# Optimization experiments

Hardware: AMD Instinct MI355X
Metric: run time of the kernel (lower is better)

The kernel has to match this reference:

```python
import jax, jax.numpy as jnp
import numpy as np

B, S, D = 8, 4096, 64

def setup_inputs() -> dict:
    key = jax.random.key(0)
    k1, k2 = jax.random.split(key)
    x = jax.random.normal(k1, (B, S, D), dtype=jnp.float32)
    y = jax.random.normal(k2, (B, S, D), dtype=jnp.float32)
    return {"x": x, "y": y}

def reference(x, y):
    # Unscaled bidirectional cross-attention.
    # m1: [B, Sx, Sy] = x @ y^T ; m2: [B, Sy, Sx] = y @ x^T (= m1^T, but keep faithful form)
    m1 = jnp.einsum('bsd,btd->bst', x, y)
    m2 = jnp.einsum('btd,bsd->bts', y, x)
    n1 = jax.nn.softmax(m1, axis=-1)
    n2 = jax.nn.softmax(m2, axis=-1)
    o1 = jnp.einsum('bst,btd->bsd', n1, y)
    o2 = jnp.einsum('bts,bsd->btd', n2, x)
    a1 = o1 * x
    a2 = o2 * y
    return jnp.concatenate((a1, a2), axis=-1)  # [B, S, 2D]
```

## Files before the change

kernel.cpp:

```cpp
#include <hip/hip_runtime.h>
#include <stdint.h>
#include <stddef.h>

#define SS 4096
#define DD 64
#define TK 64
#define NEG_M_L2 (-57.70780163555854f)
#define SQRT_L2E 1.2011224087864498f

typedef short    short4v __attribute__((ext_vector_type(4)));
typedef short    short8 __attribute__((ext_vector_type(8)));
typedef _Float16 half8  __attribute__((ext_vector_type(8)));
typedef float    f32x4  __attribute__((ext_vector_type(4)));
typedef __bf16   bf16x4v __attribute__((ext_vector_type(4)));
typedef __bf16   bf16x8v __attribute__((ext_vector_type(8)));
typedef __bf16   bf16x8 __attribute__((ext_vector_type(8)));

typedef __attribute__((address_space(1))) void void_g;
typedef __attribute__((address_space(3))) void void_l;

static __device__ __forceinline__ void gl_lds16(const void* g, void* l) {
    __builtin_amdgcn_global_load_lds((void_g*)(g), (void_l*)(l), 16, 0, 0);
}
static __device__ __forceinline__ float bf16_to_f32(unsigned short h) {
    uint32_t u = ((uint32_t)h) << 16;
    return __builtin_bit_cast(float, u);
}

#define MFMA_F16(A, B, C) __builtin_amdgcn_mfma_f32_16x16x32_f16( \
    __builtin_bit_cast(half8, A), __builtin_bit_cast(half8, B), (C), 0, 0, 0)
#define MFMA_BF16(A, B, C) __builtin_amdgcn_mfma_f32_16x16x32_bf16( \
    __builtin_bit_cast(bf16x8, A), __builtin_bit_cast(bf16x8, B), (C), 0, 0, 0)

__global__ __launch_bounds__(256) void prep(
    const float* __restrict__ x, const float* __restrict__ y,
    _Float16* __restrict__ fx, _Float16* __restrict__ fy,
    unsigned short* __restrict__ tx, unsigned short* __restrict__ ty) {
    __shared__ float tile[64 * 69];
    int bid = blockIdx.x;
    int mat = bid >> 9;
    int rem = bid & 511;
    int b = rem >> 6, t64 = rem & 63;
    int s0 = t64 * 64;
    const float* src = (mat ? y : x) + ((size_t)b * SS + s0) * 64;
    _Float16* fr = (mat ? fy : fx) + ((size_t)b * SS + s0) * 64;
    unsigned short* tr = (mat ? ty : tx) + (size_t)b * SS * 64;
    int tid = threadIdx.x;
#pragma unroll
    for (int it = 0; it < 4; ++it) {
        int qi = it * 256 + tid;
        int r = qi >> 4, c4 = (qi & 15) * 4;
        f32x4 v = *(const f32x4*)(src + r * 64 + c4);
#pragma unroll
        for (int j = 0; j < 4; ++j) tile[r * 69 + c4 + j] = v[j];
    }
#pragma unroll
    for (int j2 = 0; j2 < 2; ++j2) {
        int seg = j2 * 256 + tid;
        int r = seg >> 3, g = seg & 7;
        const float* sp8 = src + r * 64 + g * 8;
        f32x4 v0 = *(const f32x4*)(sp8);
        f32x4 v1 = *(const f32x4*)(sp8 + 4);
        half8 h;
#pragma unroll
        for (int j = 0; j < 4; ++j) {
            h[j]     = (_Float16)(v0[j] * SQRT_L2E);
            h[4 + j] = (_Float16)(v1[j] * SQRT_L2E);
        }
        *(half8*)(fr + (size_t)r * 64 + ((g + r + 2 * ((r >> 3) & 3)) & 7) * 8) = h;
    }
    __syncthreads();
#pragma unroll
    for (int j2 = 0; j2 < 2; ++j2) {
        int seg = j2 * 256 + tid;
        int d = seg >> 3, k8 = seg & 7;
        bf16x8v h;
#pragma unroll
        for (int i = 0; i < 8; ++i)
            h[i] = (__bf16)tile[(k8 * 8 + i) * 69 + d];
        *(short8*)(tr + (size_t)d * SS + s0 + ((k8 + d) & 7) * 8) =
            __builtin_bit_cast(short8, h);
    }
}

__global__ __launch_bounds__(256, 4)
void biattn(const float* __restrict__ xg, const float* __restrict__ yg,
            const _Float16* __restrict__ fx, const _Float16* __restrict__ fy,
            const unsigned short* __restrict__ tx, const unsigned short* __restrict__ ty,
            unsigned short* __restrict__ wsO, float* __restrict__ wsL,
            float* __restrict__ out, int mode) {
    __shared__ _Float16 shK[2][TK * DD];
    __shared__ unsigned short shVt[2][DD * TK];

    const int bid = blockIdx.x;
    const int g8 = bid >> 3;
    int half, bd, qb;
    qb = g8 & 31;
    if (mode) { half = (g8 >> 5) & 1; bd = (bid & 7) + 8 * (g8 >> 6); }
    else      { half = 0;             bd = (bid & 7) + 8 * (g8 >> 5); }
    const int b = bd >> 1, dir = bd & 1;
    const size_t mo = (size_t)b * SS * DD;
    const _Float16* Kf = (dir ? fx : fy) + mo;
    const unsigned short* Vt = (dir ? tx : ty) + mo;
    const _Float16* Qf = (dir ? fy : fx) + mo;
    const float* Qm = (dir ? yg : xg) + mo;

    const int tid = threadIdx.x, w = tid >> 6, ln = tid & 63;
    const int l15 = ln & 15, quad = ln >> 4;
    const int q0 = qb * 128 + w * 32;

    half8 qf[2][2];
#pragma unroll
    for (int qs = 0; qs < 2; ++qs) {
        int qrow = q0 + qs * 16 + l15;
#pragma unroll
        for (int c = 0; c < 2; ++c)
            qf[qs][c] = *(const half8*)(Qf + (size_t)qrow * 64 +
                ((c * 4 + quad + qrow + 2 * ((qrow >> 3) & 3)) & 7) * 8);
    }

    int koff[2][2][2];
#pragma unroll
    for (int c32 = 0; c32 < 2; ++c32)
#pragma unroll
        for (int st = 0; st < 2; ++st) {
            int kl = c32 * 32 + (l15 >> 2) * 8 + (l15 & 3) + st * 4;
            int rot = kl + 2 * ((kl >> 3) & 3);
#pragma unroll
            for (int c = 0; c < 2; ++c)
                koff[c32][st][c] = kl * 64 + ((c * 4 + quad + rot) & 7) * 8;
        }
    int rotv[2];
#pragma unroll
    for (int c32 = 0; c32 < 2; ++c32)
        rotv[c32] = ((c32 * 4 + quad + l15) & 7) * 8;

    const f32x4 negc4 = {NEG_M_L2, NEG_M_L2, NEG_M_L2, NEG_M_L2};
    const f32x4 zero4 = {0.f, 0.f, 0.f, 0.f};
    f32x4 Oa[2][4], La[2];
#pragma unroll
    for (int qs = 0; qs < 2; ++qs) {
        La[qs] = zero4;
#pragma unroll
        for (int dt = 0; dt < 4; ++dt) Oa[qs][dt] = zero4;
    }
    short8 onesb;
#pragma unroll
    for (int j = 0; j < 8; ++j) onesb[j] = (short)0x3F80;

    const int kblo = mode ? half * (SS / 2) : 0;
    const int kbhi = mode ? kblo + (SS / 2) : SS;

#define STAGE(BUF, KB) do {                                                   \
    _Pragma("unroll")                                                         \
    for (int i_ = 0; i_ < 4; ++i_) {                                          \
        int seg_ = w * 4 + i_;                            \
        if (seg_ < 8) {                                                       \
            gl_lds16(Kf + (size_t)(KB) * 64 + seg_ * 512 + ln * 8,            \
                     (void*)(&shK[(BUF)][0] + seg_ * 512));                   \
        } else {                                                              \
            int s2_ = seg_ - 8;                                               \
            int d_ = s2_ * 8 + (ln >> 3);                                     \
            gl_lds16(Vt + (size_t)d_ * SS + (KB) + (ln & 7) * 8,              \
                     (void*)(&shVt[(BUF)][0] + s2_ * 512));                   \
        }                                                                     \
    } } while (0)

    STAGE(0, kblo);
    __syncthreads();

    int buf = 0;
    for (int kb = kblo; kb < kbhi; kb += TK) {
        const int more = (kb + TK < kbhi);
        if (more) STAGE(buf ^ 1, kb + TK);
        const _Float16* Kb = &shK[buf][0];
        const unsigned short* Vb = &shVt[buf][0];

#pragma unroll
        for (int c32 = 0; c32 < 2; ++c32) {
            f32x4 sacc[2][2];
#pragma unroll
            for (int st = 0; st < 2; ++st) {
                half8 a0 = *(const half8*)(Kb + koff[c32][st][0]);
                half8 a1 = *(const half8*)(Kb + koff[c32][st][1]);
#pragma unroll
                for (int qs = 0; qs < 2; ++qs) {
                    f32x4 acc = MFMA_F16(a0, qf[qs][0], negc4);
                    sacc[qs][st] = MFMA_F16(a1, qf[qs][1], acc);
                }
            }
            short8 bfr[2];
#pragma unroll
            for (int qs = 0; qs < 2; ++qs) {
                bf16x8v pk;
#pragma unroll
                for (int st = 0; st < 2; ++st) {
                    f32x4 sv = sacc[qs][st];
#pragma unroll
                    for (int j = 0; j < 4; ++j)
                        pk[st * 4 + j] = (__bf16)__builtin_amdgcn_exp2f(sv[j]);
                }
                bfr[qs] = __builtin_bit_cast(short8, pk);
            }
#pragma unroll
            for (int dt = 0; dt < 4; ++dt) {
                short8 av = *(const short8*)(Vb + (dt * 16 + l15) * 64 + rotv[c32]);
                Oa[0][dt] = MFMA_BF16(av, bfr[0], Oa[0][dt]);
                Oa[1][dt] = MFMA_BF16(av, bfr[1], Oa[1][dt]);
            }
            La[0] = MFMA_BF16(onesb, bfr[0], La[0]);
            La[1] = MFMA_BF16(onesb, bfr[1], La[1]);
        }

        if (more) __syncthreads();
        buf ^= 1;
    }
#undef STAGE

    if (mode) {
        const int pb = half * 512 + bd * 32 + qb;
#pragma unroll
        for (int qs = 0; qs < 2; ++qs) {
            unsigned short* base = wsO + (size_t)pb * 8192
                                 + (size_t)(w * 2 + qs) * 1024 + l15 * 16 + quad * 4;
#pragma unroll
            for (int dt = 0; dt < 4; ++dt) {
                bf16x4v pk;
#pragma unroll
                for (int j = 0; j < 4; ++j) pk[j] = (__bf16)Oa[qs][dt][j];
                *(short4v*)(base + dt * 256) = __builtin_bit_cast(short4v, pk);
            }
            if (quad == 0)
                wsL[(size_t)pb * 128 + w * 32 + qs * 16 + l15] = La[qs][0];
        }
    } else {
#pragma unroll
        for (int qs = 0; qs < 2; ++qs) {
            float inv = 1.0f / La[qs][0];
            int qrow = q0 + qs * 16 + l15;
#pragma unroll
            for (int dt = 0; dt < 4; ++dt) {
                const float* qp = Qm + (size_t)qrow * DD + dt * 16 + quad * 4;
                f32x4 xv = *(const f32x4*)qp;
                f32x4 rr;
#pragma unroll
                for (int j = 0; j < 4; ++j) rr[j] = Oa[qs][dt][j] * inv * xv[j];
                float* op = out + ((size_t)(b * SS + qrow)) * 128 + dir * 64
                          + dt * 16 + quad * 4;
                *(f32x4*)op = rr;
            }
        }
    }
}

__global__ __launch_bounds__(256) void combine(
    const float* __restrict__ xg, const float* __restrict__ yg,
    const unsigned short* __restrict__ wsO, const float* __restrict__ wsL,
    float* __restrict__ out) {
    __shared__ float t[8 * 1088];
    int pb = blockIdx.x;
    int bd = pb >> 5, qb = pb & 31;
    int b = bd >> 1, dir = bd & 1;
    const unsigned short* p0 = wsO + (size_t)pb * 8192;
    const unsigned short* p1 = wsO + (size_t)(512 + pb) * 8192;
    const float* l0 = wsL + (size_t)pb * 128;
    const float* l1 = wsL + (size_t)(512 + pb) * 128;
    const float* Qm = (dir ? yg : xg) + (size_t)b * SS * DD;
    int tid = threadIdx.x;
#pragma unroll
    for (int j = 0; j < 8; ++j) {
        int idx = j * 1024 + tid * 4;
        short4v a = *(const short4v*)(p0 + idx);
        short4v c = *(const short4v*)(p1 + idx);
        int dt = (idx >> 8) & 3, q = (idx >> 4) & 15, dq = idx & 15;
#pragma unroll
        for (int jj = 0; jj < 4; ++jj)
            t[j * 1088 + (dt * 16 + dq + jj) * 17 + q] =
                bf16_to_f32((unsigned short)a[jj]) +
                bf16_to_f32((unsigned short)c[jj]);
    }
    __syncthreads();
    int w2 = tid >> 6, ln = tid & 63;
    int q00 = qb * 128;
#pragma unroll 4
    for (int i = 0; i < 32; ++i) {
        int q128 = w2 * 32 + i;
        int seg = q128 >> 4, lq = q128 & 15;
        float o = t[seg * 1088 + ln * 17 + lq];
        float l = l0[q128] + l1[q128];
        float qv = Qm[(size_t)(q00 + q128) * 64 + ln];
        out[((size_t)(b * SS + q00 + q128)) * 128 + dir * 64 + ln]
            = o * (1.0f / l) * qv;
    }
}

extern "C" void kernel_launch(void* const* d_in, const int* in_sizes, int n_in,
                              void* d_out, int out_size, void* d_ws, size_t ws_size,
                              hipStream_t stream) {
    const float* x = (const float*)d_in[0];
    const float* y = (const float*)d_in[1];
    char* ws = (char*)d_ws;
    const size_t MATB = (size_t)8 * SS * DD * 2;
    const size_t OSET = (size_t)1024 * 8192 * 2;
    const size_t LSET = (size_t)1024 * 128 * 4;
    _Float16* fx = (_Float16*)(ws);
    _Float16* fy = (_Float16*)(ws + MATB);
    unsigned short* tx = (unsigned short*)(ws + 2 * MATB);
    unsigned short* ty = (unsigned short*)(ws + 3 * MATB);
    unsigned short* wsO = (unsigned short*)(ws + 4 * MATB);
    float* wsL = (float*)(ws + 4 * MATB + OSET);
    const size_t need = 4 * MATB + OSET + LSET;
    const int mode = (ws_size >= need) ? 1 : 0;
    (void)in_sizes; (void)n_in; (void)out_size;
    prep<<<dim3(1024), dim3(256), 0, stream>>>(x, y, fx, fy, tx, ty);
    biattn<<<dim3(mode ? 1024 : 512), dim3(256), 0, stream>>>(
        x, y, fx, fy, tx, ty, wsO, wsL, (float*)d_out, mode);
    if (mode)
        combine<<<dim3(512), dim3(256), 0, stream>>>(x, y, wsO, wsL, (float*)d_out);
}
```

Before: 149.9 us.

## Use 512-thread blocks with 256 queries each and split keys four ways

The attention kernel now runs 8 waves per block covering 256 query rows, so each staged K/V tile is shared by twice as many queries. Keys are split into four chunks instead of two to keep the block count at 1024, and the combine kernel sums four bf16 partials and four row sums. The aim is to halve K/V staging traffic per query while keeping the GPU occupied. In exchange, the partial workspace doubles, combine reads more data, and the larger blocks may lower occupancy under the launch bound.

```diff
diff --git a/kernel.cpp b/kernel.cpp
--- a/kernel.cpp
+++ b/kernel.cpp
@@ -83,21 +83,20 @@
     }
 }
 
-__global__ __launch_bounds__(256, 4)
+__global__ __launch_bounds__(512, 4)
 void biattn(const float* __restrict__ xg, const float* __restrict__ yg,
             const _Float16* __restrict__ fx, const _Float16* __restrict__ fy,
             const unsigned short* __restrict__ tx, const unsigned short* __restrict__ ty,
             unsigned short* __restrict__ wsO, float* __restrict__ wsL,
-            float* __restrict__ out, int mode) {
+            float* __restrict__ out, int mode, int kcount) {
     __shared__ _Float16 shK[2][TK * DD];
     __shared__ unsigned short shVt[2][DD * TK];
 
     const int bid = blockIdx.x;
-    const int g8 = bid >> 3;
-    int half, bd, qb;
-    qb = g8 & 31;
-    if (mode) { half = (g8 >> 5) & 1; bd = (bid & 7) + 8 * (g8 >> 6); }
-    else      { half = 0;             bd = (bid & 7) + 8 * (g8 >> 5); }
+    const int s = mode ? (bid >> 8) : 0;
+    const int rr = bid & 255;
+    const int bd = (rr & 7) + 8 * (rr >> 7);
+    const int qt = (rr >> 3) & 15;
     const int b = bd >> 1, dir = bd & 1;
     const size_t mo = (size_t)b * SS * DD;
     const _Float16* Kf = (dir ? fx : fy) + mo;
@@ -107,7 +106,7 @@
 
     const int tid = threadIdx.x, w = tid >> 6, ln = tid & 63;
     const int l15 = ln & 15, quad = ln >> 4;
-    const int q0 = qb * 128 + w * 32;
+    const int q0 = qt * 256 + w * 32;
 
     half8 qf[2][2];
 #pragma unroll
@@ -148,13 +147,13 @@
 #pragma unroll
     for (int j = 0; j < 8; ++j) onesb[j] = (short)0x3F80;
 
-    const int kblo = mode ? half * (SS / 2) : 0;
-    const int kbhi = mode ? kblo + (SS / 2) : SS;
+    const int kblo = s * kcount;
+    const int kbhi = kblo + kcount;
 
 #define STAGE(BUF, KB) do {                                                   \
     _Pragma("unroll")                                                         \
-    for (int i_ = 0; i_ < 4; ++i_) {                                          \
-        int seg_ = w * 4 + i_;                            \
+    for (int i_ = 0; i_ < 2; ++i_) {                                          \
+        int seg_ = w * 2 + i_;                                                \
         if (seg_ < 8) {                                                       \
             gl_lds16(Kf + (size_t)(KB) * 64 + seg_ * 512 + ln * 8,            \
                      (void*)(&shK[(BUF)][0] + seg_ * 512));                   \
@@ -218,10 +217,10 @@
 #undef STAGE
 
     if (mode) {
-        const int pb = half * 512 + bd * 32 + qb;
+        const int ps = s * 256 + bd * 16 + qt;
 #pragma unroll
         for (int qs = 0; qs < 2; ++qs) {
-            unsigned short* base = wsO + (size_t)pb * 8192
+            unsigned short* base = wsO + (size_t)ps * 16384
                                  + (size_t)(w * 2 + qs) * 1024 + l15 * 16 + quad * 4;
 #pragma unroll
             for (int dt = 0; dt < 4; ++dt) {
@@ -231,7 +230,7 @@
                 *(short4v*)(base + dt * 256) = __builtin_bit_cast(short4v, pk);
             }
             if (quad == 0)
-                wsL[(size_t)pb * 128 + w * 32 + qs * 16 + l15] = La[qs][0];
+                wsL[(size_t)ps * 256 + w * 32 + qs * 16 + l15] = La[qs][0];
         }
     } else {
 #pragma unroll
@@ -242,12 +241,12 @@
             for (int dt = 0; dt < 4; ++dt) {
                 const float* qp = Qm + (size_t)qrow * DD + dt * 16 + quad * 4;
                 f32x4 xv = *(const f32x4*)qp;
-                f32x4 rr;
-#pragma unroll
-                for (int j = 0; j < 4; ++j) rr[j] = Oa[qs][dt][j] * inv * xv[j];
+                f32x4 rr2;
+#pragma unroll
+                for (int j = 0; j < 4; ++j) rr2[j] = Oa[qs][dt][j] * inv * xv[j];
                 float* op = out + ((size_t)(b * SS + qrow)) * 128 + dir * 64
                           + dt * 16 + quad * 4;
-                *(f32x4*)op = rr;
+                *(f32x4*)op = rr2;
             }
         }
     }
@@ -259,35 +258,41 @@
     float* __restrict__ out) {
     __shared__ float t[8 * 1088];
     int pb = blockIdx.x;
-    int bd = pb >> 5, qb = pb & 31;
+    int bd = pb >> 5, qb128 = pb & 31;
+    int qt = qb128 >> 1, hb = qb128 & 1;
     int b = bd >> 1, dir = bd & 1;
-    const unsigned short* p0 = wsO + (size_t)pb * 8192;
-    const unsigned short* p1 = wsO + (size_t)(512 + pb) * 8192;
-    const float* l0 = wsL + (size_t)pb * 128;
-    const float* l1 = wsL + (size_t)(512 + pb) * 128;
+    const size_t setO = (size_t)(bd * 16 + qt) * 16384 + (size_t)hb * 8192;
+    const size_t setL = (size_t)(bd * 16 + qt) * 256 + (size_t)hb * 128;
     const float* Qm = (dir ? yg : xg) + (size_t)b * SS * DD;
     int tid = threadIdx.x;
 #pragma unroll
     for (int j = 0; j < 8; ++j) {
         int idx = j * 1024 + tid * 4;
-        short4v a = *(const short4v*)(p0 + idx);
-        short4v c = *(const short4v*)(p1 + idx);
+        f32x4 a = {0.f, 0.f, 0.f, 0.f};
+#pragma unroll
+        for (int sp = 0; sp < 4; ++sp) {
+            short4v c = *(const short4v*)(wsO + (size_t)sp * 256 * 16384 + setO + idx);
+#pragma unroll
+            for (int jj = 0; jj < 4; ++jj)
+                a[jj] += bf16_to_f32((unsigned short)c[jj]);
+        }
         int dt = (idx >> 8) & 3, q = (idx >> 4) & 15, dq = idx & 15;
 #pragma unroll
         for (int jj = 0; jj < 4; ++jj)
-            t[j * 1088 + (dt * 16 + dq + jj) * 17 + q] =
-                bf16_to_f32((unsigned short)a[jj]) +
-                bf16_to_f32((unsigned short)c[jj]);
+            t[j * 1088 + (dt * 16 + dq + jj) * 17 + q] = a[jj];
     }
     __syncthreads();
     int w2 = tid >> 6, ln = tid & 63;
-    int q00 = qb * 128;
+    int q00 = qb128 * 128;
 #pragma unroll 4
     for (int i = 0; i < 32; ++i) {
         int q128 = w2 * 32 + i;
         int seg = q128 >> 4, lq = q128 & 15;
         float o = t[seg * 1088 + ln * 17 + lq];
-        float l = l0[q128] + l1[q128];
+        float l = 0.f;
+#pragma unroll
+        for (int sp = 0; sp < 4; ++sp)
+            l += wsL[(size_t)sp * 256 * 256 + setL + q128];
         float qv = Qm[(size_t)(q00 + q128) * 64 + ln];
         out[((size_t)(b * SS + q00 + q128)) * 128 + dir * 64 + ln]
             = o * (1.0f / l) * qv;
@@ -301,8 +306,8 @@
     const float* y = (const float*)d_in[1];
     char* ws = (char*)d_ws;
     const size_t MATB = (size_t)8 * SS * DD * 2;
-    const size_t OSET = (size_t)1024 * 8192 * 2;
-    const size_t LSET = (size_t)1024 * 128 * 4;
+    const size_t OSET = (size_t)1024 * 16384 * 2;
+    const size_t LSET = (size_t)1024 * 256 * 4;
     _Float16* fx = (_Float16*)(ws);
     _Float16* fy = (_Float16*)(ws + MATB);
     unsigned short* tx = (unsigned short*)(ws + 2 * MATB);
@@ -313,8 +318,9 @@
     const int mode = (ws_size >= need) ? 1 : 0;
     (void)in_sizes; (void)n_in; (void)out_size;
     prep<<<dim3(1024), dim3(256), 0, stream>>>(x, y, fx, fy, tx, ty);
-    biattn<<<dim3(mode ? 1024 : 512), dim3(256), 0, stream>>>(
-        x, y, fx, fy, tx, ty, wsO, wsL, (float*)d_out, mode);
+    biattn<<<dim3(mode ? 1024 : 256), dim3(512), 0, stream>>>(
+        x, y, fx, fy, tx, ty, wsO, wsL, (float*)d_out, mode,
+        mode ? (SS / 4) : SS);
     if (mode)
         combine<<<dim3(512), dim3(256), 0, stream>>>(x, y, wsO, wsL, (float*)d_out);
 }
```

After: 149.0 us. Within noise of the previous version (-0.6%).
